# Optimization experiments

Measured on AMD Instinct MI355X. Metric: run time of the kernel, lower is better.

Reference implementation:

```python
import jax, jax.numpy as jnp
import numpy as np

N, E, H, G = 50000, 800000, 256, 50
CUTOFF = 10.0
PI = float(np.pi)
LOG2 = float(np.log(2.0))

def ssp(x):
    # ShiftedSoftplus: softplus(x) - log(2)
    return jax.nn.softplus(x) - LOG2

def setup_inputs() -> dict:
    key = jax.random.key(0)
    ks = jax.random.split(key, 16)
    def lin(kw, kb, fan_in, fan_out):
        s = float(np.sqrt(6.0 / (fan_in + fan_out)))  # xavier_uniform
        W = jax.random.uniform(kw, (fan_in, fan_out), minval=-s, maxval=s, dtype=jnp.float32)
        b = jnp.zeros((fan_out,), jnp.float32)
        return W, b
    h = jax.random.normal(ks[0], (N, H), dtype=jnp.float32)
    edge_index = jax.random.randint(ks[1], (2, E), 0, N, dtype=jnp.int64)
    edge_weight = jax.random.uniform(ks[2], (E,), dtype=jnp.float32) * CUTOFF
    edge_attr = jax.random.normal(ks[3], (E, G), dtype=jnp.float32)
    aw_W, aw_b = lin(ks[4], ks[5], H, H)   # atom_wise
    m1_W, m1_b = lin(ks[6], ks[7], G, H)   # mlp[0]
    m2_W, m2_b = lin(ks[8], ks[9], H, H)   # mlp[2] (num_filters == hidden)
    o1_W, o1_b = lin(ks[10], ks[11], H, H) # out[0]
    o2_W, o2_b = lin(ks[12], ks[13], H, H) # out[2]
    return {"h": h, "edge_index": edge_index, "edge_weight": edge_weight,
            "edge_attr": edge_attr, "aw_W": aw_W, "aw_b": aw_b,
            "m1_W": m1_W, "m1_b": m1_b, "m2_W": m2_W, "m2_b": m2_b,
            "o1_W": o1_W, "o1_b": o1_b, "o2_W": o2_W, "o2_b": o2_b}

def reference(h, edge_index, edge_weight, edge_attr,
              aw_W, aw_b, m1_W, m1_b, m2_W, m2_b,
              o1_W, o1_b, o2_W, o2_b):
    n_nodes = h.shape[0]
    # atom-wise linear
    h1 = h @ aw_W + aw_b                                   # [N, H]
    # cosine cutoff per edge
    C = 0.5 * (jnp.cos(edge_weight * (PI / CUTOFF)) + 1.0) # [E]
    # edge filter MLP on RBF features
    Wf = ssp(ssp(edge_attr @ m1_W + m1_b) @ m2_W + m2_b)   # [E, H]
    Wf = Wf * C[:, None]
    # CFConv: gather x_j, modulate, scatter-add to target nodes
    src, dst = edge_index[0], edge_index[1]
    msg = h1[src] * Wf                                     # [E, H]
    agg = jax.ops.segment_sum(msg, dst, num_segments=n_nodes)
    # output MLP
    out = ssp(agg @ o1_W + o1_b) @ o2_W + o2_b             # [N, H]
    return out
```

## Files before the change

kernel.cpp:

```cpp
#include <hip/hip_runtime.h>

#define N_NODES 50000
#define N_EDGES 800000

typedef __attribute__((ext_vector_type(8))) short bf16x8;
typedef __attribute__((ext_vector_type(4))) float f32x4;
typedef __attribute__((ext_vector_type(2))) float f32x2;
typedef __attribute__((ext_vector_type(4))) unsigned int u32x4;

__device__ __forceinline__ float bf2f(unsigned int u) {
  union { unsigned int u; float f; } c; c.u = (u & 0xffffu) << 16; return c.f;
}
__device__ __forceinline__ unsigned short f2bf(float f) {
  union { float f; unsigned int u; } c; c.f = f;
  return (unsigned short)((c.u + 0x8000u) >> 16);
}
__device__ __forceinline__ unsigned int pk_bf16(float lo, float hi) {
  unsigned int r;
  asm("v_cvt_pk_bf16_f32 %0, %1, %2" : "=v"(r) : "v"(lo), "v"(hi));
  return r;
}

#if __has_builtin(__builtin_amdgcn_exp2f) && __has_builtin(__builtin_amdgcn_logf)
__device__ __forceinline__ float sspf(float x) {
  const float e = __builtin_amdgcn_exp2f(fabsf(x) * -1.44269504088896f);
  const float l = __builtin_amdgcn_logf(1.0f + e);
  return fmaf(0.69314718055994531f, l, fmaxf(x, 0.0f) - 0.69314718055994531f);
}
#else
__device__ __forceinline__ float sspf(float x) {
  return fmaxf(x, 0.0f) + __logf(1.0f + __expf(-fabsf(x))) - 0.69314718055994531f;
}
#endif

__device__ __forceinline__ f32x4 MFMA(bf16x8 a, bf16x8 b, f32x4 c) {
  return __builtin_amdgcn_mfma_f32_16x16x32_bf16(a, b, c, 0, 0, 0);
}
__device__ __forceinline__ f32x4 f4bcast(float v) {
  f32x4 z = {v, v, v, v}; return z;
}

__device__ __forceinline__ bf16x8 cvt8pk(const float* __restrict__ p) {
  f32x4 x0 = *(const f32x4*)p;
  f32x4 x1 = *(const f32x4*)(p + 4);
  union { u32x4 u; bf16x8 v; } r;
  r.u[0] = pk_bf16(x0[0], x0[1]);
  r.u[1] = pk_bf16(x0[2], x0[3]);
  r.u[2] = pk_bf16(x1[0], x1[1]);
  r.u[3] = pk_bf16(x1[2], x1[3]);
  return r.v;
}

template<int ADT, int ACT, int ODT>
__global__ __launch_bounds__(512, 8) void gemm512(
    const void* __restrict__ Av, const unsigned short* __restrict__ Wt,
    const float* __restrict__ bias, void* __restrict__ Outv, int M)
{
  __shared__ unsigned short a_lds[64 * 256];
  const int m0  = (int)blockIdx.x * 64;
  const int tid = (int)threadIdx.x;

  {
    const int r   = tid >> 3;
    const int oc8 = tid & 7;
    int row = m0 + r;
    if (row >= M) row = M - 1;
    if (ADT == 1) {
      const float* ap = (const float*)Av + (size_t)row * 256 + oc8 * 32;
#pragma unroll
      for (int q = 0; q < 4; ++q) {
        const bf16x8 v = cvt8pk(ap + q * 8);
        const int byt = r * 512 + ((oc8 * 64 + q * 16) ^ ((r & 7) << 4));
        *(bf16x8*)((char*)a_lds + byt) = v;
      }
    } else {
      const unsigned short* ap =
          (const unsigned short*)Av + (size_t)row * 256 + oc8 * 32;
#pragma unroll
      for (int q = 0; q < 4; ++q) {
        const bf16x8 v = *(const bf16x8*)(ap + q * 8);
        const int byt = r * 512 + ((oc8 * 64 + q * 16) ^ ((r & 7) << 4));
        *(bf16x8*)((char*)a_lds + byt) = v;
      }
    }
  }
  __syncthreads();

  const int w  = tid >> 6, l = tid & 63, lr = l & 15, g = l >> 4;
  const int c0 = w * 32;
  const int P45 = (lr & 3) << 4;
  const int P6  = (lr & 4) << 4;
  const int alb = lr * 512 + ((g * 16) ^ P45);

  const float bs0 = bias[c0 + lr];
  const float bs1 = bias[c0 + 16 + lr];
  f32x4 acc[4][2];
#pragma unroll
  for (int a = 0; a < 4; ++a) {
    acc[a][0] = f4bcast(bs0);
    acc[a][1] = f4bcast(bs1);
  }

#pragma unroll
  for (int ks = 0; ks < 8; ++ks) {
    const int kb = ks * 32 + g * 8;
    const bf16x8 bfr0 = *(const bf16x8*)(Wt + (size_t)(c0 + lr) * 256 + kb);
    const bf16x8 bfr1 = *(const bf16x8*)(Wt + (size_t)(c0 + 16 + lr) * 256 + kb);
    const char* abase = (const char*)a_lds + (alb + ((ks * 64) ^ P6));
#pragma unroll
    for (int mf = 0; mf < 4; ++mf) {
      const bf16x8 af = *(const bf16x8*)(abase + mf * 8192);
      __builtin_amdgcn_s_setprio(1);
      acc[mf][0] = MFMA(af, bfr0, acc[mf][0]);
      acc[mf][1] = MFMA(af, bfr1, acc[mf][1]);
      __builtin_amdgcn_s_setprio(0);
    }
  }

#pragma unroll
  for (int nf = 0; nf < 2; ++nf) {
    const int col = c0 + nf * 16 + lr;
#pragma unroll
    for (int mf = 0; mf < 4; ++mf) {
#pragma unroll
      for (int i = 0; i < 4; ++i) {
        const int row = m0 + mf * 16 + g * 4 + i;
        if (row < M) {
          float x = acc[mf][nf][i];
          if (ACT) x = sspf(x);
          if (ODT == 0)
            ((unsigned short*)Outv)[(size_t)row * 256 + col] = f2bf(x);
          else
            ((float*)Outv)[(size_t)row * 256 + col] = x;
        }
      }
    }
  }
}

__global__ __launch_bounds__(512, 8) void out_fused512(
    const float* __restrict__ agg,
    const unsigned short* __restrict__ o1t, const float* __restrict__ o1b,
    const unsigned short* __restrict__ o2t, const float* __restrict__ o2b,
    float* __restrict__ Out, int M)
{
  __shared__ unsigned short t_lds[64 * 256];
  const int m0  = (int)blockIdx.x * 64;
  const int tid = (int)threadIdx.x;

  {
    const int r   = tid >> 3;
    const int oc8 = tid & 7;
    int row = m0 + r;
    if (row >= M) row = M - 1;
    const float* ap = agg + (size_t)row * 256 + oc8 * 32;
#pragma unroll
    for (int q = 0; q < 4; ++q) {
      const bf16x8 v = cvt8pk(ap + q * 8);
      const int byt = r * 512 + ((oc8 * 64 + q * 16) ^ ((r & 7) << 4));
      *(bf16x8*)((char*)t_lds + byt) = v;
    }
  }
  __syncthreads();

  const int w  = tid >> 6, l = tid & 63, lr = l & 15, g = l >> 4;
  const int c0 = w * 32;
  const int P45 = (lr & 3) << 4;
  const int P6  = (lr & 4) << 4;
  const int alb = lr * 512 + ((g * 16) ^ P45);

  f32x4 acc[4][2];
  {
    const float b0 = o1b[c0 + lr];
    const float b1 = o1b[c0 + 16 + lr];
#pragma unroll
    for (int a = 0; a < 4; ++a) {
      acc[a][0] = f4bcast(b0);
      acc[a][1] = f4bcast(b1);
    }
  }

#pragma unroll
  for (int ks = 0; ks < 8; ++ks) {
    const int kb = ks * 32 + g * 8;
    const bf16x8 bfr0 = *(const bf16x8*)(o1t + (size_t)(c0 + lr) * 256 + kb);
    const bf16x8 bfr1 = *(const bf16x8*)(o1t + (size_t)(c0 + 16 + lr) * 256 + kb);
    const char* abase = (const char*)t_lds + (alb + ((ks * 64) ^ P6));
#pragma unroll
    for (int mf = 0; mf < 4; ++mf) {
      const bf16x8 af = *(const bf16x8*)(abase + mf * 8192);
      __builtin_amdgcn_s_setprio(1);
      acc[mf][0] = MFMA(af, bfr0, acc[mf][0]);
      acc[mf][1] = MFMA(af, bfr1, acc[mf][1]);
      __builtin_amdgcn_s_setprio(0);
    }
  }
  __syncthreads();

#pragma unroll
  for (int nf = 0; nf < 2; ++nf) {
    const int colb = (c0 + nf * 16 + lr) * 2;
#pragma unroll
    for (int i = 0; i < 4; ++i) {
      const int gi = g * 4 + i;
      char* wp = (char*)t_lds + (gi * 512 + (colb ^ ((gi & 7) << 4)));
      const float v0 = sspf(acc[0][nf][i]);
      const float v1 = sspf(acc[1][nf][i]);
      const float v2 = sspf(acc[2][nf][i]);
      const float v3 = sspf(acc[3][nf][i]);
      const unsigned int p01 = pk_bf16(v0, v1);
      const unsigned int p23 = pk_bf16(v2, v3);
      *(unsigned short*)(wp)         = (unsigned short)p01;
      *(unsigned short*)(wp + 8192)  = (unsigned short)(p01 >> 16);
      *(unsigned short*)(wp + 16384) = (unsigned short)p23;
      *(unsigned short*)(wp + 24576) = (unsigned short)(p23 >> 16);
    }
  }
  __syncthreads();

  {
    const float b0 = o2b[c0 + lr];
    const float b1 = o2b[c0 + 16 + lr];
#pragma unroll
    for (int a = 0; a < 4; ++a) {
      acc[a][0] = f4bcast(b0);
      acc[a][1] = f4bcast(b1);
    }
  }
#pragma unroll
  for (int ks = 0; ks < 8; ++ks) {
    const int kb = ks * 32 + g * 8;
    const bf16x8 bfr0 = *(const bf16x8*)(o2t + (size_t)(c0 + lr) * 256 + kb);
    const bf16x8 bfr1 = *(const bf16x8*)(o2t + (size_t)(c0 + 16 + lr) * 256 + kb);
    const char* abase = (const char*)t_lds + (alb + ((ks * 64) ^ P6));
#pragma unroll
    for (int mf = 0; mf < 4; ++mf) {
      const bf16x8 af = *(const bf16x8*)(abase + mf * 8192);
      __builtin_amdgcn_s_setprio(1);
      acc[mf][0] = MFMA(af, bfr0, acc[mf][0]);
      acc[mf][1] = MFMA(af, bfr1, acc[mf][1]);
      __builtin_amdgcn_s_setprio(0);
    }
  }

#pragma unroll
  for (int nf = 0; nf < 2; ++nf) {
    const int col = c0 + nf * 16 + lr;
#pragma unroll
    for (int mf = 0; mf < 4; ++mf) {
#pragma unroll
      for (int i = 0; i < 4; ++i) {
        const int row = m0 + mf * 16 + g * 4 + i;
        if (row < M)
          Out[(size_t)row * 256 + col] = acc[mf][nf][i];
      }
    }
  }
}

__global__ __launch_bounds__(256) void hist_dst(const int* __restrict__ eidx,
                                                int* __restrict__ cnt)
{
  const int e = (int)blockIdx.x * 256 + (int)threadIdx.x;
  atomicAdd(&cnt[eidx[N_EDGES + e]], 1);
}

__global__ __launch_bounds__(1024) void scan_cnt(const int* __restrict__ cnt,
                                                 int* __restrict__ cursor)
{
  __shared__ int part[1024];
  const int t = (int)threadIdx.x;
  const int base = t * 49;
  int s = 0;
#pragma unroll 7
  for (int j = 0; j < 49; ++j) {
    const int idx = base + j;
    if (idx < N_NODES) s += cnt[idx];
  }
  part[t] = s;
  __syncthreads();
  for (int off = 1; off < 1024; off <<= 1) {
    int v = 0;
    if (t >= off) v = part[t - off];
    __syncthreads();
    part[t] += v;
    __syncthreads();
  }
  int run = (t == 0) ? 0 : part[t - 1];
#pragma unroll 7
  for (int j = 0; j < 49; ++j) {
    const int idx = base + j;
    if (idx < N_NODES) { cursor[idx] = run; run += cnt[idx]; }
  }
}

__global__ __launch_bounds__(256) void scatter_perm(
    const int* __restrict__ eidx, const float* __restrict__ ew,
    int* __restrict__ cursor, int* __restrict__ perm,
    float* __restrict__ Cf, int* __restrict__ srcs, int* __restrict__ dsts)
{
  const int e = (int)blockIdx.x * 256 + (int)threadIdx.x;
  const int d = eidx[N_EDGES + e];
  const int pos = atomicAdd(&cursor[d], 1);
  perm[pos] = e;
  Cf[pos]   = 0.5f * (__cosf(ew[e] * 0.31415926535897931f) + 1.0f);
  srcs[pos] = eidx[e];
  dsts[pos] = d;
}

__global__ __launch_bounds__(512, 8) void edge_fused512(
    const float* __restrict__ eattr, const int* __restrict__ perm,
    const float* __restrict__ Cf,
    const int* __restrict__ srcs, const int* __restrict__ dsts,
    const unsigned short* __restrict__ m1t, const float* __restrict__ m1b,
    const unsigned short* __restrict__ m2t, const float* __restrict__ m2b,
    const unsigned short* __restrict__ h1, float* __restrict__ agg)
{
  __shared__ unsigned short t_lds[64 * 256];
  __shared__ float Cs[64];
  __shared__ int s_src[64];
  __shared__ int s_dst[65];
  unsigned short* ea_lds = t_lds;

  const int e0  = (int)blockIdx.x * 64;
  const int tid = (int)threadIdx.x;

  {
    const int r  = tid >> 3;
    const int oc = tid & 7;
    const int p  = perm[e0 + r];
    const float* ap = eattr + (size_t)p * 50 + oc * 8;
    union { u32x4 u; bf16x8 v; } t;
    if (oc < 6) {
      f32x2 a0 = *(const f32x2*)(ap);
      f32x2 a1 = *(const f32x2*)(ap + 2);
      f32x2 a2 = *(const f32x2*)(ap + 4);
      f32x2 a3 = *(const f32x2*)(ap + 6);
      t.u[0] = pk_bf16(a0[0], a0[1]);
      t.u[1] = pk_bf16(a1[0], a1[1]);
      t.u[2] = pk_bf16(a2[0], a2[1]);
      t.u[3] = pk_bf16(a3[0], a3[1]);
    } else if (oc == 6) {
      f32x2 a0 = *(const f32x2*)(ap);
      t.u[0] = pk_bf16(a0[0], a0[1]);
      t.u[1] = 0; t.u[2] = 0; t.u[3] = 0;
    } else {
      t.u[0] = 0; t.u[1] = 0; t.u[2] = 0; t.u[3] = 0;
    }
    const int byt = r * 128 + ((oc * 16) ^ ((r & 7) << 4));
    *(bf16x8*)((char*)ea_lds + byt) = t.v;
  }
  if (tid < 64) {
    Cs[tid]    = Cf[e0 + tid];
    s_src[tid] = srcs[e0 + tid];
    s_dst[tid] = dsts[e0 + tid];
  }
  if (tid == 64)
    s_dst[64] = (e0 + 64 < N_EDGES) ? dsts[e0 + 64] : -1;
  __syncthreads();

  const int w  = tid >> 6;
  const int l  = tid & 63;
  const int lr = l & 15;
  const int g  = l >> 4;
  const int c0 = w * 32;

  const int P45  = (lr & 3) << 4;
  const int P6   = (lr & 4) << 4;
  const int alb1 = lr * 128 + ((g * 16) ^ P45);
  const int alb2 = lr * 512 + ((g * 16) ^ P45);

  const float b10 = m1b[c0 + lr];
  const float b11 = m1b[c0 + 16 + lr];
  f32x4 acc[4][2];
#pragma unroll
  for (int a = 0; a < 4; ++a) {
    acc[a][0] = f4bcast(b10);
    acc[a][1] = f4bcast(b11);
  }

#pragma unroll
  for (int ks = 0; ks < 2; ++ks) {
    const int kb = ks * 32 + g * 8;
    const bf16x8 bfr0 = *(const bf16x8*)(m1t + (c0 + lr) * 64 + kb);
    const bf16x8 bfr1 = *(const bf16x8*)(m1t + (c0 + 16 + lr) * 64 + kb);
    const char* abase = (const char*)ea_lds + (alb1 + ((ks * 64) ^ P6));
#pragma unroll
    for (int mf = 0; mf < 4; ++mf) {
      const bf16x8 af = *(const bf16x8*)(abase + mf * 2048);
      __builtin_amdgcn_s_setprio(1);
      acc[mf][0] = MFMA(af, bfr0, acc[mf][0]);
      acc[mf][1] = MFMA(af, bfr1, acc[mf][1]);
      __builtin_amdgcn_s_setprio(0);
    }
  }
  __syncthreads();

#pragma unroll
  for (int nf = 0; nf < 2; ++nf) {
    const int colb = (c0 + nf * 16 + lr) * 2;
#pragma unroll
    for (int i = 0; i < 4; ++i) {
      const int gi = g * 4 + i;
      char* wp = (char*)t_lds + (gi * 512 + (colb ^ ((gi & 7) << 4)));
      const float v0 = sspf(acc[0][nf][i]);
      const float v1 = sspf(acc[1][nf][i]);
      const float v2 = sspf(acc[2][nf][i]);
      const float v3 = sspf(acc[3][nf][i]);
      const unsigned int p01 = pk_bf16(v0, v1);
      const unsigned int p23 = pk_bf16(v2, v3);
      *(unsigned short*)(wp)         = (unsigned short)p01;
      *(unsigned short*)(wp + 8192)  = (unsigned short)(p01 >> 16);
      *(unsigned short*)(wp + 16384) = (unsigned short)p23;
      *(unsigned short*)(wp + 24576) = (unsigned short)(p23 >> 16);
    }
  }
  __syncthreads();

  const float b20 = m2b[c0 + lr];
  const float b21 = m2b[c0 + 16 + lr];
#pragma unroll
  for (int a = 0; a < 4; ++a) {
    acc[a][0] = f4bcast(b20);
    acc[a][1] = f4bcast(b21);
  }

#pragma unroll
  for (int ks = 0; ks < 8; ++ks) {
    const int kb = ks * 32 + g * 8;
    const bf16x8 bfr0 = *(const bf16x8*)(m2t + (size_t)(c0 + lr) * 256 + kb);
    const bf16x8 bfr1 = *(const bf16x8*)(m2t + (size_t)(c0 + 16 + lr) * 256 + kb);
    const char* abase = (const char*)t_lds + (alb2 + ((ks * 64) ^ P6));
#pragma unroll
    for (int mf = 0; mf < 4; ++mf) {
      const bf16x8 af = *(const bf16x8*)(abase + mf * 8192);
      __builtin_amdgcn_s_setprio(1);
      acc[mf][0] = MFMA(af, bfr0, acc[mf][0]);
      acc[mf][1] = MFMA(af, bfr1, acc[mf][1]);
      __builtin_amdgcn_s_setprio(0);
    }
  }
  __syncthreads();

#pragma unroll
  for (int nf = 0; nf < 2; ++nf) {
    const int colb = (c0 + nf * 16 + lr) * 2;
#pragma unroll
    for (int i = 0; i < 4; ++i) {
      const int gi = g * 4 + i;
      char* wp = (char*)t_lds + (gi * 512 + (colb ^ ((gi & 7) << 4)));
      const float v0 = sspf(acc[0][nf][i]) * Cs[gi];
      const float v1 = sspf(acc[1][nf][i]) * Cs[16 + gi];
      const float v2 = sspf(acc[2][nf][i]) * Cs[32 + gi];
      const float v3 = sspf(acc[3][nf][i]) * Cs[48 + gi];
      const unsigned int p01 = pk_bf16(v0, v1);
      const unsigned int p23 = pk_bf16(v2, v3);
      *(unsigned short*)(wp)         = (unsigned short)p01;
      *(unsigned short*)(wp + 8192)  = (unsigned short)(p01 >> 16);
      *(unsigned short*)(wp + 16384) = (unsigned short)p23;
      *(unsigned short*)(wp + 24576) = (unsigned short)(p23 >> 16);
    }
  }
  __syncthreads();

  {
    const int q2 = tid >> 7;
    const int cp = (tid & 127) * 2;
    const int rb = q2 * 16;
    float s0 = 0.f, s1 = 0.f;
#pragma unroll
    for (int rr = 0; rr < 16; ++rr) {
      const int r = rb + rr;
      const int byt = r * 512 + ((cp * 2) ^ ((r & 7) << 4));
      const unsigned int wfp = *(const unsigned int*)((const char*)t_lds + byt);
      const unsigned int xjp =
          *(const unsigned int*)(h1 + (size_t)s_src[r] * 256 + cp);
      s0 += bf2f(wfp) * bf2f(xjp);
      s1 += bf2f(wfp >> 16) * bf2f(xjp >> 16);
      const int d = s_dst[r];
      if (rr == 15 || s_dst[r + 1] != d) {
        float* ap = agg + (size_t)d * 256 + cp;
        atomicAdd(ap, s0);
        atomicAdd(ap + 1, s1);
        s0 = 0.f; s1 = 0.f;
      }
    }
  }
}

__global__ __launch_bounds__(256) void prep_weights(
    const float* __restrict__ aw, const float* __restrict__ m1,
    const float* __restrict__ m2, const float* __restrict__ o1,
    const float* __restrict__ o2,
    unsigned short* __restrict__ awt, unsigned short* __restrict__ m1t,
    unsigned short* __restrict__ m2t, unsigned short* __restrict__ o1t,
    unsigned short* __restrict__ o2t)
{
  const int i = (int)blockIdx.x * 256 + (int)threadIdx.x;
  const int c = i >> 8, k = i & 255;
  const int src = k * 256 + c;
  awt[i] = f2bf(aw[src]);
  m2t[i] = f2bf(m2[src]);
  o1t[i] = f2bf(o1[src]);
  o2t[i] = f2bf(o2[src]);
  if (k < 64) m1t[c * 64 + k] = (k < 50) ? f2bf(m1[k * 256 + c]) : (unsigned short)0;
}

extern "C" void kernel_launch(void* const* d_in, const int* in_sizes, int n_in,
                              void* d_out, int out_size, void* d_ws, size_t ws_size,
                              hipStream_t stream)
{
  const float* h    = (const float*)d_in[0];
  const int*   eidx = (const int*)d_in[1];
  const float* ew   = (const float*)d_in[2];
  const float* ea   = (const float*)d_in[3];
  const float* awW  = (const float*)d_in[4];
  const float* awb  = (const float*)d_in[5];
  const float* m1W  = (const float*)d_in[6];
  const float* m1b  = (const float*)d_in[7];
  const float* m2W  = (const float*)d_in[8];
  const float* m2b  = (const float*)d_in[9];
  const float* o1W  = (const float*)d_in[10];
  const float* o1b  = (const float*)d_in[11];
  const float* o2W  = (const float*)d_in[12];
  const float* o2b  = (const float*)d_in[13];

  char* ws = (char*)d_ws;
  unsigned short* h1  = (unsigned short*)ws;
  float*          agg = (float*)(ws + 25600000);
  char* wbase = ws + 25600000 + 51200000;
  unsigned short* awt = (unsigned short*)wbase;
  unsigned short* m2t = awt + 65536;
  unsigned short* o1t = m2t + 65536;
  unsigned short* o2t = o1t + 65536;
  unsigned short* m1t = o2t + 65536;
  char* p0 = wbase + 4 * 131072 + 32768;
  int* cnt    = (int*)p0;
  int* cursor = cnt + N_NODES;
  int* perm   = cursor + N_NODES;
  char* p1 = p0 + 400000 + 3200000;
  float* Cf   = (float*)p1;
  int*   srcs = (int*)(p1 + 3200000);
  int*   dsts = (int*)(p1 + 6400000);

  hipMemsetAsync(agg, 0, (size_t)N_NODES * 256 * 4, stream);
  hipMemsetAsync(cnt, 0, (size_t)N_NODES * 4, stream);

  prep_weights<<<256, 256, 0, stream>>>(awW, m1W, m2W, o1W, o2W,
                                        awt, m1t, m2t, o1t, o2t);
  hist_dst<<<N_EDGES / 256, 256, 0, stream>>>(eidx, cnt);
  scan_cnt<<<1, 1024, 0, stream>>>(cnt, cursor);
  scatter_perm<<<N_EDGES / 256, 256, 0, stream>>>(eidx, ew, cursor, perm,
                                                  Cf, srcs, dsts);

  gemm512<1, 0, 0><<<(N_NODES + 63) / 64, 512, 0, stream>>>(h, awt, awb, h1, N_NODES);

  edge_fused512<<<N_EDGES / 64, 512, 0, stream>>>(
      ea, perm, Cf, srcs, dsts, m1t, m1b, m2t, m2b, h1, agg);

  out_fused512<<<(N_NODES + 63) / 64, 512, 0, stream>>>(
      agg, o1t, o1b, o2t, o2b, (float*)d_out, N_NODES);
}
```

Before: 689.9 us.

## Process two edge tiles per block and prefetch second tile's inputs during first

The fused edge kernel now handles 128 edges per block as two 64-edge tiles. The gather of the second tile's edge attributes and its metadata is issued into registers during the first tile's second GEMM, so the global-load latency can overlap with MFMA work. The grid is halved, which lowers parallelism and raises register pressure from the prefetched values.

```diff
diff --git a/kernel.cpp b/kernel.cpp
--- a/kernel.cpp
+++ b/kernel.cpp
@@ -49,6 +49,32 @@
   r.u[2] = pk_bf16(x1[0], x1[1]);
   r.u[3] = pk_bf16(x1[2], x1[3]);
   return r.v;
+}
+
+__device__ __forceinline__ bf16x8 gather_ea(
+    const float* __restrict__ eattr, const int* __restrict__ perm,
+    int e0, int gr, int goc)
+{
+  const int p = perm[e0 + gr];
+  const float* ap = eattr + (size_t)p * 50 + goc * 8;
+  union { u32x4 u; bf16x8 v; } t;
+  if (goc < 6) {
+    f32x2 a0 = *(const f32x2*)(ap);
+    f32x2 a1 = *(const f32x2*)(ap + 2);
+    f32x2 a2 = *(const f32x2*)(ap + 4);
+    f32x2 a3 = *(const f32x2*)(ap + 6);
+    t.u[0] = pk_bf16(a0[0], a0[1]);
+    t.u[1] = pk_bf16(a1[0], a1[1]);
+    t.u[2] = pk_bf16(a2[0], a2[1]);
+    t.u[3] = pk_bf16(a3[0], a3[1]);
+  } else if (goc == 6) {
+    f32x2 a0 = *(const f32x2*)(ap);
+    t.u[0] = pk_bf16(a0[0], a0[1]);
+    t.u[1] = 0; t.u[2] = 0; t.u[3] = 0;
+  } else {
+    t.u[0] = 0; t.u[1] = 0; t.u[2] = 0; t.u[3] = 0;
+  }
+  return t.v;
 }
 
 template<int ADT, int ACT, int ODT>
@@ -322,151 +348,125 @@
   __shared__ int s_dst[65];
   unsigned short* ea_lds = t_lds;
 
-  const int e0  = (int)blockIdx.x * 64;
   const int tid = (int)threadIdx.x;
-
-  {
-    const int r  = tid >> 3;
-    const int oc = tid & 7;
-    const int p  = perm[e0 + r];
-    const float* ap = eattr + (size_t)p * 50 + oc * 8;
-    union { u32x4 u; bf16x8 v; } t;
-    if (oc < 6) {
-      f32x2 a0 = *(const f32x2*)(ap);
-      f32x2 a1 = *(const f32x2*)(ap + 2);
-      f32x2 a2 = *(const f32x2*)(ap + 4);
-      f32x2 a3 = *(const f32x2*)(ap + 6);
-      t.u[0] = pk_bf16(a0[0], a0[1]);
-      t.u[1] = pk_bf16(a1[0], a1[1]);
-      t.u[2] = pk_bf16(a2[0], a2[1]);
-      t.u[3] = pk_bf16(a3[0], a3[1]);
-    } else if (oc == 6) {
-      f32x2 a0 = *(const f32x2*)(ap);
-      t.u[0] = pk_bf16(a0[0], a0[1]);
-      t.u[1] = 0; t.u[2] = 0; t.u[3] = 0;
-    } else {
-      t.u[0] = 0; t.u[1] = 0; t.u[2] = 0; t.u[3] = 0;
-    }
-    const int byt = r * 128 + ((oc * 16) ^ ((r & 7) << 4));
-    *(bf16x8*)((char*)ea_lds + byt) = t.v;
-  }
-  if (tid < 64) {
-    Cs[tid]    = Cf[e0 + tid];
-    s_src[tid] = srcs[e0 + tid];
-    s_dst[tid] = dsts[e0 + tid];
-  }
-  if (tid == 64)
-    s_dst[64] = (e0 + 64 < N_EDGES) ? dsts[e0 + 64] : -1;
-  __syncthreads();
+  const int e0A = (int)blockIdx.x * 128;
+  const int e0B = e0A + 64;
+
+  const int gr   = tid >> 3;
+  const int goc  = tid & 7;
+  const int gbyt = gr * 128 + ((goc * 16) ^ ((gr & 7) << 4));
 
   const int w  = tid >> 6;
   const int l  = tid & 63;
   const int lr = l & 15;
   const int g  = l >> 4;
   const int c0 = w * 32;
-
   const int P45  = (lr & 3) << 4;
   const int P6   = (lr & 4) << 4;
   const int alb1 = lr * 128 + ((g * 16) ^ P45);
   const int alb2 = lr * 512 + ((g * 16) ^ P45);
-
   const float b10 = m1b[c0 + lr];
   const float b11 = m1b[c0 + 16 + lr];
-  f32x4 acc[4][2];
-#pragma unroll
-  for (int a = 0; a < 4; ++a) {
-    acc[a][0] = f4bcast(b10);
-    acc[a][1] = f4bcast(b11);
-  }
-
-#pragma unroll
-  for (int ks = 0; ks < 2; ++ks) {
-    const int kb = ks * 32 + g * 8;
-    const bf16x8 bfr0 = *(const bf16x8*)(m1t + (c0 + lr) * 64 + kb);
-    const bf16x8 bfr1 = *(const bf16x8*)(m1t + (c0 + 16 + lr) * 64 + kb);
-    const char* abase = (const char*)ea_lds + (alb1 + ((ks * 64) ^ P6));
-#pragma unroll
-    for (int mf = 0; mf < 4; ++mf) {
-      const bf16x8 af = *(const bf16x8*)(abase + mf * 2048);
-      __builtin_amdgcn_s_setprio(1);
-      acc[mf][0] = MFMA(af, bfr0, acc[mf][0]);
-      acc[mf][1] = MFMA(af, bfr1, acc[mf][1]);
-      __builtin_amdgcn_s_setprio(0);
-    }
-  }
-  __syncthreads();
-
-#pragma unroll
-  for (int nf = 0; nf < 2; ++nf) {
-    const int colb = (c0 + nf * 16 + lr) * 2;
-#pragma unroll
-    for (int i = 0; i < 4; ++i) {
-      const int gi = g * 4 + i;
-      char* wp = (char*)t_lds + (gi * 512 + (colb ^ ((gi & 7) << 4)));
-      const float v0 = sspf(acc[0][nf][i]);
-      const float v1 = sspf(acc[1][nf][i]);
-      const float v2 = sspf(acc[2][nf][i]);
-      const float v3 = sspf(acc[3][nf][i]);
-      const unsigned int p01 = pk_bf16(v0, v1);
-      const unsigned int p23 = pk_bf16(v2, v3);
-      *(unsigned short*)(wp)         = (unsigned short)p01;
-      *(unsigned short*)(wp + 8192)  = (unsigned short)(p01 >> 16);
-      *(unsigned short*)(wp + 16384) = (unsigned short)p23;
-      *(unsigned short*)(wp + 24576) = (unsigned short)(p23 >> 16);
-    }
-  }
-  __syncthreads();
-
   const float b20 = m2b[c0 + lr];
   const float b21 = m2b[c0 + 16 + lr];
-#pragma unroll
-  for (int a = 0; a < 4; ++a) {
-    acc[a][0] = f4bcast(b20);
-    acc[a][1] = f4bcast(b21);
-  }
-
-#pragma unroll
-  for (int ks = 0; ks < 8; ++ks) {
-    const int kb = ks * 32 + g * 8;
-    const bf16x8 bfr0 = *(const bf16x8*)(m2t + (size_t)(c0 + lr) * 256 + kb);
-    const bf16x8 bfr1 = *(const bf16x8*)(m2t + (size_t)(c0 + 16 + lr) * 256 + kb);
-    const char* abase = (const char*)t_lds + (alb2 + ((ks * 64) ^ P6));
-#pragma unroll
-    for (int mf = 0; mf < 4; ++mf) {
-      const bf16x8 af = *(const bf16x8*)(abase + mf * 8192);
-      __builtin_amdgcn_s_setprio(1);
-      acc[mf][0] = MFMA(af, bfr0, acc[mf][0]);
-      acc[mf][1] = MFMA(af, bfr1, acc[mf][1]);
-      __builtin_amdgcn_s_setprio(0);
-    }
-  }
-  __syncthreads();
-
-#pragma unroll
-  for (int nf = 0; nf < 2; ++nf) {
-    const int colb = (c0 + nf * 16 + lr) * 2;
-#pragma unroll
-    for (int i = 0; i < 4; ++i) {
-      const int gi = g * 4 + i;
-      char* wp = (char*)t_lds + (gi * 512 + (colb ^ ((gi & 7) << 4)));
-      const float v0 = sspf(acc[0][nf][i]) * Cs[gi];
-      const float v1 = sspf(acc[1][nf][i]) * Cs[16 + gi];
-      const float v2 = sspf(acc[2][nf][i]) * Cs[32 + gi];
-      const float v3 = sspf(acc[3][nf][i]) * Cs[48 + gi];
-      const unsigned int p01 = pk_bf16(v0, v1);
-      const unsigned int p23 = pk_bf16(v2, v3);
-      *(unsigned short*)(wp)         = (unsigned short)p01;
-      *(unsigned short*)(wp + 8192)  = (unsigned short)(p01 >> 16);
-      *(unsigned short*)(wp + 16384) = (unsigned short)p23;
-      *(unsigned short*)(wp + 24576) = (unsigned short)(p23 >> 16);
-    }
-  }
-  __syncthreads();
-
-  {
-    const int q2 = tid >> 7;
-    const int cp = (tid & 127) * 2;
-    const int rb = q2 * 16;
+
+  const int q2 = tid >> 7;
+  const int cp = (tid & 127) * 2;
+  const int rb = q2 * 16;
+
+  f32x4 acc[4][2];
+
+  auto stage1 = [&]() {
+#pragma unroll
+    for (int a = 0; a < 4; ++a) {
+      acc[a][0] = f4bcast(b10);
+      acc[a][1] = f4bcast(b11);
+    }
+#pragma unroll
+    for (int ks = 0; ks < 2; ++ks) {
+      const int kb = ks * 32 + g * 8;
+      const bf16x8 bfr0 = *(const bf16x8*)(m1t + (c0 + lr) * 64 + kb);
+      const bf16x8 bfr1 = *(const bf16x8*)(m1t + (c0 + 16 + lr) * 64 + kb);
+      const char* abase = (const char*)ea_lds + (alb1 + ((ks * 64) ^ P6));
+#pragma unroll
+      for (int mf = 0; mf < 4; ++mf) {
+        const bf16x8 af = *(const bf16x8*)(abase + mf * 2048);
+        __builtin_amdgcn_s_setprio(1);
+        acc[mf][0] = MFMA(af, bfr0, acc[mf][0]);
+        acc[mf][1] = MFMA(af, bfr1, acc[mf][1]);
+        __builtin_amdgcn_s_setprio(0);
+      }
+    }
+  };
+
+  auto ep1 = [&]() {
+#pragma unroll
+    for (int nf = 0; nf < 2; ++nf) {
+      const int colb = (c0 + nf * 16 + lr) * 2;
+#pragma unroll
+      for (int i = 0; i < 4; ++i) {
+        const int gi = g * 4 + i;
+        char* wp = (char*)t_lds + (gi * 512 + (colb ^ ((gi & 7) << 4)));
+        const float v0 = sspf(acc[0][nf][i]);
+        const float v1 = sspf(acc[1][nf][i]);
+        const float v2 = sspf(acc[2][nf][i]);
+        const float v3 = sspf(acc[3][nf][i]);
+        const unsigned int p01 = pk_bf16(v0, v1);
+        const unsigned int p23 = pk_bf16(v2, v3);
+        *(unsigned short*)(wp)         = (unsigned short)p01;
+        *(unsigned short*)(wp + 8192)  = (unsigned short)(p01 >> 16);
+        *(unsigned short*)(wp + 16384) = (unsigned short)p23;
+        *(unsigned short*)(wp + 24576) = (unsigned short)(p23 >> 16);
+      }
+    }
+  };
+
+  auto stage2 = [&]() {
+#pragma unroll
+    for (int a = 0; a < 4; ++a) {
+      acc[a][0] = f4bcast(b20);
+      acc[a][1] = f4bcast(b21);
+    }
+#pragma unroll
+    for (int ks = 0; ks < 8; ++ks) {
+      const int kb = ks * 32 + g * 8;
+      const bf16x8 bfr0 = *(const bf16x8*)(m2t + (size_t)(c0 + lr) * 256 + kb);
+      const bf16x8 bfr1 = *(const bf16x8*)(m2t + (size_t)(c0 + 16 + lr) * 256 + kb);
+      const char* abase = (const char*)t_lds + (alb2 + ((ks * 64) ^ P6));
+#pragma unroll
+      for (int mf = 0; mf < 4; ++mf) {
+        const bf16x8 af = *(const bf16x8*)(abase + mf * 8192);
+        __builtin_amdgcn_s_setprio(1);
+        acc[mf][0] = MFMA(af, bfr0, acc[mf][0]);
+        acc[mf][1] = MFMA(af, bfr1, acc[mf][1]);
+        __builtin_amdgcn_s_setprio(0);
+      }
+    }
+  };
+
+  auto ep2 = [&]() {
+#pragma unroll
+    for (int nf = 0; nf < 2; ++nf) {
+      const int colb = (c0 + nf * 16 + lr) * 2;
+#pragma unroll
+      for (int i = 0; i < 4; ++i) {
+        const int gi = g * 4 + i;
+        char* wp = (char*)t_lds + (gi * 512 + (colb ^ ((gi & 7) << 4)));
+        const float v0 = sspf(acc[0][nf][i]) * Cs[gi];
+        const float v1 = sspf(acc[1][nf][i]) * Cs[16 + gi];
+        const float v2 = sspf(acc[2][nf][i]) * Cs[32 + gi];
+        const float v3 = sspf(acc[3][nf][i]) * Cs[48 + gi];
+        const unsigned int p01 = pk_bf16(v0, v1);
+        const unsigned int p23 = pk_bf16(v2, v3);
+        *(unsigned short*)(wp)         = (unsigned short)p01;
+        *(unsigned short*)(wp + 8192)  = (unsigned short)(p01 >> 16);
+        *(unsigned short*)(wp + 16384) = (unsigned short)p23;
+        *(unsigned short*)(wp + 24576) = (unsigned short)(p23 >> 16);
+      }
+    }
+  };
+
+  auto reduceA = [&]() {
     float s0 = 0.f, s1 = 0.f;
 #pragma unroll
     for (int rr = 0; rr < 16; ++rr) {
@@ -485,7 +485,62 @@
         s0 = 0.f; s1 = 0.f;
       }
     }
-  }
+  };
+
+  {
+    const bf16x8 gA = gather_ea(eattr, perm, e0A, gr, goc);
+    if (tid < 64) {
+      Cs[tid]    = Cf[e0A + tid];
+      s_src[tid] = srcs[e0A + tid];
+      s_dst[tid] = dsts[e0A + tid];
+    }
+    if (tid == 64) s_dst[64] = dsts[e0B];
+    *(bf16x8*)((char*)ea_lds + gbyt) = gA;
+  }
+  __syncthreads();
+
+  stage1();
+  __syncthreads();
+  ep1();
+  __syncthreads();
+  stage2();
+
+  const bf16x8 gB = gather_ea(eattr, perm, e0B, gr, goc);
+  float cB = 0.f; int srB = 0, dB = 0, dEndB = 0;
+  if (tid < 64) {
+    cB  = Cf[e0B + tid];
+    srB = srcs[e0B + tid];
+    dB  = dsts[e0B + tid];
+  }
+  if (tid == 64)
+    dEndB = (e0B + 64 < N_EDGES) ? dsts[e0B + 64] : -1;
+
+  __syncthreads();
+  ep2();
+  __syncthreads();
+  reduceA();
+  __syncthreads();
+
+  {
+    if (tid < 64) {
+      Cs[tid]    = cB;
+      s_src[tid] = srB;
+      s_dst[tid] = dB;
+    }
+    if (tid == 64) s_dst[64] = dEndB;
+    *(bf16x8*)((char*)ea_lds + gbyt) = gB;
+  }
+  __syncthreads();
+
+  stage1();
+  __syncthreads();
+  ep1();
+  __syncthreads();
+  stage2();
+  __syncthreads();
+  ep2();
+  __syncthreads();
+  reduceA();
 }
 
 __global__ __launch_bounds__(256) void prep_weights(
@@ -555,7 +610,7 @@
 
   gemm512<1, 0, 0><<<(N_NODES + 63) / 64, 512, 0, stream>>>(h, awt, awb, h1, N_NODES);
 
-  edge_fused512<<<N_EDGES / 64, 512, 0, stream>>>(
+  edge_fused512<<<N_EDGES / 128, 512, 0, stream>>>(
       ea, perm, Cf, srcs, dsts, m1t, m1b, m2t, m2b, h1, agg);
 
   out_fused512<<<(N_NODES + 63) / 64, 512, 0, stream>>>(
```

After: 1.000 ms. 45.0% more time.
